# Optimization experiments

Measured on AMD Instinct MI355X. Metric: run time of the kernel, lower is better.

Reference implementation:

```python
import jax, jax.numpy as jnp
import numpy as np

WS = 7            # window size
NUM_HEADS = 16
DIM = 512
B_ = 4096         # num_windows * batch
NW = 1024         # windows per image
N = WS * WS


def _relative_position_index(ws=WS):
    # static int index table, computed exactly as in the torch module
    coords = np.stack(np.meshgrid(np.arange(ws), np.arange(ws), indexing='ij'))  # (2, ws, ws)
    coords = coords.reshape(2, -1)                                               # (2, N)
    rel = coords[:, :, None] - coords[:, None, :]                                # (2, N, N)
    rel = rel.transpose(1, 2, 0).astype(np.int64)                                # (N, N, 2)
    rel[:, :, 0] += ws - 1
    rel[:, :, 1] += ws - 1
    rel[:, :, 0] *= 2 * ws - 1
    return jnp.asarray(rel.sum(-1))                                              # (N, N)


def setup_inputs() -> dict:
    key = jax.random.key(0)
    ks = jax.random.split(key, 12)
    C = DIM
    std = 0.02
    inp = {
        'local_features': jax.random.normal(ks[0], (B_, N, C), jnp.float32),
        'global_features': jax.random.normal(ks[1], (B_, N, C), jnp.float32),
        'mask': jnp.zeros((NW, N, N), jnp.float32),  # 0/-inf shifted-window mask (all-visible here)
        'bias_table': std * jax.random.normal(ks[2], ((2 * WS - 1) * (2 * WS - 1), NUM_HEADS), jnp.float32),
        'Wk': std * jax.random.normal(ks[3], (C, C), jnp.float32),
        'bk': jnp.zeros((C,), jnp.float32),
        'Wq': std * jax.random.normal(ks[4], (C, C), jnp.float32),
        'bq': jnp.zeros((C,), jnp.float32),
        'Wv': std * jax.random.normal(ks[5], (C, C), jnp.float32),
        'bv': jnp.zeros((C,), jnp.float32),
        'Wp': std * jax.random.normal(ks[6], (C, C), jnp.float32),
        'bp': jnp.zeros((C,), jnp.float32),
    }
    return inp


def reference(local_features, global_features, mask, bias_table,
              Wk, bk, Wq, bq, Wv, bv, Wp, bp):
    Bw, n, C = local_features.shape
    h = NUM_HEADS
    d = C // h
    scale = d ** -0.5

    def heads(x, W, b):
        # torch Linear: x @ W.T + b ; then (B_, N, h, d) -> (B_, h, N, d)
        y = jnp.einsum('bnc,oc->bno', x, W) + b
        return y.reshape(Bw, n, h, d).transpose(0, 2, 1, 3)

    k = heads(local_features, Wk, bk)
    q = heads(global_features, Wq, bq) * scale
    v = heads(local_features, Wv, bv)

    attn = jnp.einsum('bhnd,bhmd->bhnm', q, k)                    # (B_, h, N, N)

    idx = _relative_position_index()                               # (N, N) static
    rpb = bias_table[idx]                                          # (N, N, h)
    attn = attn + rpb.transpose(2, 0, 1)[None]                     # add (1, h, N, N)

    nW = mask.shape[0]
    attn = attn.reshape(Bw // nW, nW, h, n, n) + mask[None, :, None]
    attn = attn.reshape(Bw, h, n, n)
    attn = jax.nn.softmax(attn, axis=-1)

    x = jnp.einsum('bhnm,bhmd->bnhd', attn, v).reshape(Bw, n, C)
    x = jnp.einsum('bnc,oc->bno', x, Wp) + bp
    return x
```

## Files before the change

### kernel.cpp

```cpp
#include <hip/hip_runtime.h>
#include <hip/hip_bf16.h>

typedef __hip_bfloat16 bf16;
typedef __attribute__((ext_vector_type(4))) float f32x4;
typedef __attribute__((ext_vector_type(8))) short short8;
typedef __attribute__((ext_vector_type(4))) short short4v;

#define NEGBIG (-3.0e38f)

__device__ __forceinline__ unsigned short f2b(float x) {
  union { float f; unsigned int u; } v; v.f = x;
  unsigned int r = v.u + 0x7fffu + ((v.u >> 16) & 1u);
  return (unsigned short)(r >> 16);
}

__device__ __forceinline__ void gl16(const void* g, void* l) {
  __builtin_amdgcn_global_load_lds(
      (const __attribute__((address_space(1))) unsigned int*)g,
      (__attribute__((address_space(3))) unsigned int*)l, 16, 0, 0);
}

__device__ __forceinline__ int xcd_swz(int orig, int nwg) {
  const int q = nwg >> 3, r = nwg & 7;
  const int xcd = orig & 7;
  const int base = (xcd < r) ? xcd * (q + 1) : r * (q + 1) + (xcd - r) * q;
  return base + (orig >> 3);
}

__global__ __launch_bounds__(256) void cvt_w_kernel(
    const float* __restrict__ a, const float* __restrict__ b,
    const float* __restrict__ c, const float* __restrict__ d,
    bf16* __restrict__ dst) {
  const int t = blockIdx.x * 256 + threadIdx.x;
  const float* srcs[4] = {a, b, c, d};
#pragma unroll
  for (int w = 0; w < 4; ++w) {
    const f32x4 v = *(const f32x4*)(srcs[w] + (size_t)t * 4);
    short4v o;
    o[0] = (short)f2b(v[0]); o[1] = (short)f2b(v[1]);
    o[2] = (short)f2b(v[2]); o[3] = (short)f2b(v[3]);
    *(short4v*)((short*)dst + (size_t)w * 262144 + (size_t)t * 4) = o;
  }
}

__global__ __launch_bounds__(256) void cvt_a(const float* __restrict__ src,
                                             short* __restrict__ dst, int M) {
  const int g = blockIdx.x * 256 + threadIdx.x;
  const int row = g >> 6, k8 = g & 63;
  if (row >= M) return;
  const float* sp = src + (size_t)row * 512 + k8 * 8;
  const f32x4 lo = *(const f32x4*)sp;
  const f32x4 hi = *(const f32x4*)(sp + 4);
  short8 u;
  u[0] = (short)f2b(lo[0]); u[1] = (short)f2b(lo[1]);
  u[2] = (short)f2b(lo[2]); u[3] = (short)f2b(lo[3]);
  u[4] = (short)f2b(hi[0]); u[5] = (short)f2b(hi[1]);
  u[6] = (short)f2b(hi[2]); u[7] = (short)f2b(hi[3]);
  *(short8*)(dst + (size_t)row * 512 + k8 * 8) = u;
}

__global__ __launch_bounds__(256) void prep_rpbL(const float* __restrict__ btab,
                                                 float* __restrict__ rpbL) {
  const int g = blockIdx.x * 256 + threadIdx.x;
  const int lane = g & 63, mn = (g >> 6) & 15, h = g >> 10;
  const int m = mn >> 2, n = mn & 3, l15 = lane & 15, lg = lane >> 4;
  const int cc = n * 16 + l15;
  const int aj = cc / 7, bj = cc % 7;
  f32x4 o;
#pragma unroll
  for (int reg = 0; reg < 4; ++reg) {
    const int i = m * 16 + lg * 4 + reg;
    if (i < 49 && cc < 49) {
      const int t = (i / 7 - aj + 6) * 13 + (i % 7 - bj + 6);
      o[reg] = btab[t * 16 + h];
    } else {
      o[reg] = NEGBIG;
    }
  }
  ((f32x4*)rpbL)[g] = o;
}

__global__ __launch_bounds__(256) void prep_maskL(const float* __restrict__ mask,
                                                  float* __restrict__ maskL) {
  const int g = blockIdx.x * 256 + threadIdx.x;
  const int lane = g & 63, mn = (g >> 6) & 15, wm = g >> 10;
  const int m = mn >> 2, n = mn & 3, l15 = lane & 15, lg = lane >> 4;
  const int cc = n * 16 + l15;
  f32x4 o;
#pragma unroll
  for (int reg = 0; reg < 4; ++reg) {
    const int i = m * 16 + lg * 4 + reg;
    o[reg] = (i < 49 && cc < 49) ? mask[(size_t)wm * 2401 + i * 49 + cc] : 0.f;
  }
  ((f32x4*)maskL)[g] = o;
}

__device__ __forceinline__ void stage_m97(const char* Ab, const char* Bb,
                                          char* As, char* Bs, int arow0,
                                          int brow0, int k0) {
  const int tid = threadIdx.x;
#pragma unroll
  for (int i = 0; i < 2; ++i) {
    const int s = tid + 512 * i;
    const int row = s >> 3;
    const int sc = (s & 7) ^ (row & 7);
    gl16(Ab + (size_t)(arow0 + row) * 1024 + k0 * 2 + sc * 16, As + s * 16);
  }
#pragma unroll
  for (int i = 0; i < 4; ++i) {
    const int s = tid + 512 * i;
    const int row = s >> 3;
    const int sc = (s & 7) ^ (row & 7);
    gl16(Bb + (size_t)(brow0 + row) * 1024 + k0 * 2 + sc * 16, Bs + s * 16);
  }
}

__global__ __launch_bounds__(512, 4) void gemm_kqv(
    const short* __restrict__ Al, const short* __restrict__ Ag,
    const short* __restrict__ wbf, const float* __restrict__ bk,
    const float* __restrict__ bq, const float* __restrict__ bv, float qscale,
    bf16* __restrict__ k_ws, bf16* __restrict__ q_ws, bf16* __restrict__ vT_ws,
    int M) {
  __shared__ char lds[49152];
  char* As = lds;
  char* Bs = lds + 16384;
  const int nwg = gridDim.x;
  const int t0 = xcd_swz(blockIdx.x, nwg);
  const int bn = t0 % 6, bm = t0 / 6;
  const int cls = bn >> 1, bnl = bn & 1;
  const int tid = threadIdx.x, lane = tid & 63, wid = tid >> 6;
  const int l15 = lane & 15, lg = lane >> 4;
  const bool swap = (cls == 2);
  const int wr = swap ? (wid & 3) : (wid >> 2);
  const int wc = swap ? (wid >> 2) : (wid & 3);
  const char* Ab = (const char*)((cls == 1) ? Ag : Al);
  const char* Bb = (const char*)(wbf + (size_t)cls * 262144);

  f32x4 acc[4][4];
#pragma unroll
  for (int m = 0; m < 4; ++m)
#pragma unroll
    for (int n = 0; n < 4; ++n) acc[m][n] = (f32x4){0.f, 0.f, 0.f, 0.f};

  const char* fam = swap ? Bs : As;
  const char* fbm = swap ? As : Bs;

  for (int kt = 0; kt < 8; ++kt) {
    stage_m97(Ab, Bb, As, Bs, bm * 128, bnl * 256, kt * 64);
    __syncthreads();
#pragma unroll
    for (int s = 0; s < 2; ++s) {
      short8 af[4], bfr[4];
#pragma unroll
      for (int m = 0; m < 4; ++m) {
        const int r = wr * 64 + m * 16 + l15;
        af[m] = *(const short8*)(fam + r * 128 +
                                 (((s * 4 + lg) ^ (r & 7)) << 4));
      }
#pragma unroll
      for (int n = 0; n < 4; ++n) {
        const int r = wc * 64 + n * 16 + l15;
        bfr[n] = *(const short8*)(fbm + r * 128 +
                                  (((s * 4 + lg) ^ (r & 7)) << 4));
      }
#pragma unroll
      for (int m = 0; m < 4; ++m)
#pragma unroll
        for (int n = 0; n < 4; ++n)
          acc[m][n] = __builtin_amdgcn_mfma_f32_16x16x32_bf16(
              af[m], bfr[n], acc[m][n], 0, 0, 0);
    }
    __syncthreads();
  }

  if (cls == 2) {
#pragma unroll
    for (int m = 0; m < 4; ++m) {
#pragma unroll
      for (int n = 0; n < 4; ++n) {
        const int tok = bm * 128 + wc * 64 + n * 16 + l15;
        if (tok < M) {
          const int w = tok / 49, nt = tok - w * 49;
#pragma unroll
          for (int reg = 0; reg < 4; ++reg) {
            const int ch = bnl * 256 + wr * 64 + m * 16 + lg * 4 + reg;
            const float v = acc[m][n][reg] + bv[ch];
            const int hh = ch >> 5, dd = ch & 31;
            vT_ws[(((size_t)w * 16 + hh) * 32 + dd) * 64 + nt] =
                __float2bfloat16(v);
          }
        }
      }
    }
  } else {
    const float* bb = (cls == 0) ? bk : bq;
    bf16* dp = (cls == 0) ? k_ws : q_ws;
    const float sc = (cls == 0) ? 1.0f : qscale;
#pragma unroll
    for (int m = 0; m < 4; ++m) {
#pragma unroll
      for (int n = 0; n < 4; ++n) {
        const int c = bnl * 256 + wc * 64 + n * 16 + l15;
        const float bvv = bb[c];
        const int hh = c >> 5, dd = c & 31;
#pragma unroll
        for (int reg = 0; reg < 4; ++reg) {
          const int r = bm * 128 + wr * 64 + m * 16 + lg * 4 + reg;
          if (r < M) {
            const int w = r / 49, nt = r - w * 49;
            dp[(((size_t)w * 16 + hh) * 49 + nt) * 32 + dd] =
                __float2bfloat16((acc[m][n][reg] + bvv) * sc);
          }
        }
      }
    }
  }
}

__global__ __launch_bounds__(512, 4) void gemm_p(const short* __restrict__ Abf,
                                                 const short* __restrict__ Bbf,
                                                 const float* __restrict__ bias,
                                                 float* __restrict__ dst,
                                                 int M) {
  __shared__ char lds[49152];
  char* As = lds;
  char* Bs = lds + 16384;
  const int nwg = gridDim.x;
  const int t0 = xcd_swz(blockIdx.x, nwg);
  const int bnl = t0 & 1, bm = t0 >> 1;
  const int tid = threadIdx.x, lane = tid & 63, wid = tid >> 6;
  const int wr = wid >> 2, wc = wid & 3, l15 = lane & 15, lg = lane >> 4;

  f32x4 acc[4][4];
#pragma unroll
  for (int m = 0; m < 4; ++m)
#pragma unroll
    for (int n = 0; n < 4; ++n) acc[m][n] = (f32x4){0.f, 0.f, 0.f, 0.f};

  for (int kt = 0; kt < 8; ++kt) {
    stage_m97((const char*)Abf, (const char*)Bbf, As, Bs, bm * 128, bnl * 256,
              kt * 64);
    __syncthreads();
#pragma unroll
    for (int s = 0; s < 2; ++s) {
      short8 af[4], bfr[4];
#pragma unroll
      for (int m = 0; m < 4; ++m) {
        const int r = wr * 64 + m * 16 + l15;
        af[m] = *(const short8*)(As + r * 128 +
                                 (((s * 4 + lg) ^ (r & 7)) << 4));
      }
#pragma unroll
      for (int n = 0; n < 4; ++n) {
        const int r = wc * 64 + n * 16 + l15;
        bfr[n] = *(const short8*)(Bs + r * 128 +
                                  (((s * 4 + lg) ^ (r & 7)) << 4));
      }
#pragma unroll
      for (int m = 0; m < 4; ++m)
#pragma unroll
        for (int n = 0; n < 4; ++n)
          acc[m][n] = __builtin_amdgcn_mfma_f32_16x16x32_bf16(
              af[m], bfr[n], acc[m][n], 0, 0, 0);
    }
    __syncthreads();
  }

#pragma unroll
  for (int m = 0; m < 4; ++m) {
#pragma unroll
    for (int n = 0; n < 4; ++n) {
      const int c = bnl * 256 + wc * 64 + n * 16 + l15;
      const float bvv = bias[c];
#pragma unroll
      for (int reg = 0; reg < 4; ++reg) {
        const int r = bm * 128 + wr * 64 + m * 16 + lg * 4 + reg;
        if (r < M) dst[(size_t)r * 512 + c] = acc[m][n][reg] + bvv;
      }
    }
  }
}

__global__ __launch_bounds__(256) void attn_win2(
    const bf16* __restrict__ q_ws, const bf16* __restrict__ k_ws,
    const bf16* __restrict__ vT_ws, const float* __restrict__ rpbL,
    const float* __restrict__ maskL, bf16* __restrict__ x_ws, int wstart) {
  __shared__ short sP[4][4096];
  const int tid = threadIdx.x, lane = tid & 63, wid = tid >> 6;
  const int l15 = lane & 15, lg = lane >> 4;
  const int wl = blockIdx.x;
  const int h = blockIdx.y * 4 + wid;
  const int wg = wstart + wl;
  char* Pl = (char*)sP[wid];
  const size_t base = ((size_t)wl * 16 + h) * 1568;
  const short8 z8 = (short8){0, 0, 0, 0, 0, 0, 0, 0};

  short8 qf[4], kf[4];
#pragma unroll
  for (int m = 0; m < 4; ++m) {
    const int r = m * 16 + l15;
    qf[m] = (r < 49) ? *(const short8*)(q_ws + base + r * 32 + lg * 8) : z8;
    kf[m] = (r < 49) ? *(const short8*)(k_ws + base + r * 32 + lg * 8) : z8;
  }
  f32x4 lc[4][4];
#pragma unroll
  for (int m = 0; m < 4; ++m)
#pragma unroll
    for (int n = 0; n < 4; ++n)
      lc[m][n] = __builtin_amdgcn_mfma_f32_16x16x32_bf16(
          qf[m], kf[n], (f32x4){0.f, 0.f, 0.f, 0.f}, 0, 0, 0);

  const f32x4* rbp = (const f32x4*)rpbL + (size_t)h * 1024 + lane;
  const f32x4* mkp = (const f32x4*)maskL + (size_t)(wg & 1023) * 1024 + lane;
#pragma unroll
  for (int m = 0; m < 4; ++m)
#pragma unroll
    for (int n = 0; n < 4; ++n) {
      const int mn = m * 4 + n;
      lc[m][n] += rbp[mn * 64] + mkp[mn * 64];
    }

#pragma unroll
  for (int m = 0; m < 4; ++m) {
#pragma unroll
    for (int reg = 0; reg < 4; ++reg) {
      float vmax = fmaxf(fmaxf(lc[m][0][reg], lc[m][1][reg]),
                         fmaxf(lc[m][2][reg], lc[m][3][reg]));
#pragma unroll
      for (int off = 1; off < 16; off <<= 1)
        vmax = fmaxf(vmax, __shfl_xor(vmax, off, 64));
      float e[4], ssum = 0.f;
#pragma unroll
      for (int n = 0; n < 4; ++n) {
        e[n] = __expf(lc[m][n][reg] - vmax);
        ssum += e[n];
      }
#pragma unroll
      for (int off = 1; off < 16; off <<= 1) ssum += __shfl_xor(ssum, off, 64);
      const float inv = __builtin_amdgcn_rcpf(ssum);
      const int i = m * 16 + lg * 4 + reg;
#pragma unroll
      for (int n = 0; n < 4; ++n) {
        const int cc = n * 16 + l15;
        *(unsigned short*)(Pl + i * 128 + ((2 * cc) ^ ((i & 7) << 4))) =
            f2b(e[n] * inv);
      }
    }
  }

  f32x4 xacc[4][2];
#pragma unroll
  for (int m = 0; m < 4; ++m)
#pragma unroll
    for (int n = 0; n < 2; ++n) xacc[m][n] = (f32x4){0.f, 0.f, 0.f, 0.f};
  const size_t vbase = ((size_t)wl * 16 + h) * 2048;
#pragma unroll
  for (int s = 0; s < 2; ++s) {
    short8 pf[4], vf[2];
#pragma unroll
    for (int m = 0; m < 4; ++m) {
      const int i = m * 16 + l15;
      pf[m] = *(const short8*)(Pl + i * 128 +
                               ((s * 64 + lg * 16) ^ ((i & 7) << 4)));
    }
#pragma unroll
    for (int n = 0; n < 2; ++n) {
      const int dd = n * 16 + l15;
      short8 vv = *(const short8*)(vT_ws + vbase + dd * 64 + s * 32 + lg * 8);
      if (s == 1) {
        if (lg == 3) vv = z8;
        else if (lg == 2) {
          vv[1] = 0; vv[2] = 0; vv[3] = 0; vv[4] = 0;
          vv[5] = 0; vv[6] = 0; vv[7] = 0;
        }
      }
      vf[n] = vv;
    }
#pragma unroll
    for (int m = 0; m < 4; ++m)
#pragma unroll
      for (int n = 0; n < 2; ++n)
        xacc[m][n] = __builtin_amdgcn_mfma_f32_16x16x32_bf16(
            pf[m], vf[n], xacc[m][n], 0, 0, 0);
  }

#pragma unroll
  for (int m = 0; m < 4; ++m)
#pragma unroll
    for (int n = 0; n < 2; ++n)
#pragma unroll
      for (int reg = 0; reg < 4; ++reg) {
        const int i = m * 16 + lg * 4 + reg;
        const int dd = n * 16 + l15;
        *(unsigned short*)(Pl + i * 80 + ((2 * dd) ^ ((i & 3) << 4))) =
            f2b(xacc[m][n][reg]);
      }
#pragma unroll
  for (int g = 0; g < 4; ++g) {
    const int row = g * 16 + (lane >> 2);
    if (row < 49) {
      const short8 xv = *(const short8*)(
          Pl + row * 80 + (((lane & 3) * 16) ^ ((row & 3) << 4)));
      *(short8*)(x_ws + ((size_t)wl * 49 + row) * 512 + h * 32 +
                 (lane & 3) * 8) = xv;
    }
  }
}

extern "C" void kernel_launch(void* const* d_in, const int* in_sizes, int n_in,
                              void* d_out, int out_size, void* d_ws,
                              size_t ws_size, hipStream_t stream) {
  const float* lf   = (const float*)d_in[0];
  const float* gfx  = (const float*)d_in[1];
  const float* mask = (const float*)d_in[2];
  const float* btab = (const float*)d_in[3];
  const float* Wk = (const float*)d_in[4];  const float* bk = (const float*)d_in[5];
  const float* Wq = (const float*)d_in[6];  const float* bq = (const float*)d_in[7];
  const float* Wv = (const float*)d_in[8];  const float* bv = (const float*)d_in[9];
  const float* Wp = (const float*)d_in[10]; const float* bp = (const float*)d_in[11];
  float* out = (float*)d_out;

  char* ws = (char*)d_ws;
  short* wbf = (short*)ws;
  size_t off = (size_t)4 * 262144 * 2;
  float* rpbL = (float*)(ws + off); off += (size_t)16 * 4096 * 4;
  float* maskL = (float*)(ws + off); off += (size_t)1024 * 4096 * 4;

  const size_t perw = 2 * 49 * 1024 + 2 * 50176 + 65536;
  size_t avail = (ws_size > off + 65536) ? ws_size - off - 65536 : 0;
  int CH = (int)((avail > 300000) ? (avail - 262144) / perw : 1);
  if (CH > 4096) CH = 4096;
  if (CH < 1) CH = 1;
  const int RWS = ((CH * 49 + 127) / 128) * 128;

  short* Al = (short*)(ws + off); off += (size_t)RWS * 1024;
  short* Ag = (short*)(ws + off); off += (size_t)RWS * 1024;
  bf16* q_ws = (bf16*)(ws + off); off += (size_t)CH * 50176;
  bf16* k_ws = (bf16*)(ws + off); off += (size_t)CH * 50176;
  bf16* vT_ws = (bf16*)(ws + off); off += (size_t)CH * 65536;
  bf16* x_ws = (bf16*)Al;

  cvt_w_kernel<<<256, 256, 0, stream>>>(Wk, Wq, Wv, Wp, (bf16*)wbf);
  prep_rpbL<<<64, 256, 0, stream>>>(btab, rpbL);
  prep_maskL<<<4096, 256, 0, stream>>>(mask, maskL);

  const float qscale = 0.17677669529663687f;
  for (int wstart = 0; wstart < 4096; wstart += CH) {
    const int nwin = (4096 - wstart < CH) ? (4096 - wstart) : CH;
    const int M = nwin * 49;
    const int gy = (M + 127) / 128;
    const int cg = (M * 64 + 255) / 256;
    cvt_a<<<cg, 256, 0, stream>>>(lf + (size_t)wstart * 25088, Al, M);
    cvt_a<<<cg, 256, 0, stream>>>(gfx + (size_t)wstart * 25088, Ag, M);
    gemm_kqv<<<6 * gy, 512, 0, stream>>>(Al, Ag, wbf, bk, bq, bv, qscale,
                                         k_ws, q_ws, vT_ws, M);
    attn_win2<<<dim3(nwin, 4), 256, 0, stream>>>(q_ws, k_ws, vT_ws, rpbL,
                                                 maskL, x_ws, wstart);
    gemm_p<<<2 * gy, 512, 0, stream>>>((const short*)x_ws, wbf + 3 * 262144,
                                       bp, out + (size_t)wstart * 25088, M);
  }
}
```

Before: 1.271 ms.

## Fuse fp32-to-bf16 activation conversion into the QKV GEMM staging

Drops the separate cvt_a passes over local and global features. The QKV GEMM now loads fp32 activation tiles into LDS, converts them to bf16 with packed convert instructions, and writes them into the swizzled layout before running the MFMA loop. This removes a full write and read of bf16 copies of both inputs through global memory. In exchange, LDS per block grows to 80KB, each k-step gains an extra barrier, and each activation tile is re-read and re-converted by all six column blocks.

```diff
diff --git a/kernel.cpp b/kernel.cpp
--- a/kernel.cpp
+++ b/kernel.cpp
@@ -41,22 +41,6 @@
     o[2] = (short)f2b(v[2]); o[3] = (short)f2b(v[3]);
     *(short4v*)((short*)dst + (size_t)w * 262144 + (size_t)t * 4) = o;
   }
-}
-
-__global__ __launch_bounds__(256) void cvt_a(const float* __restrict__ src,
-                                             short* __restrict__ dst, int M) {
-  const int g = blockIdx.x * 256 + threadIdx.x;
-  const int row = g >> 6, k8 = g & 63;
-  if (row >= M) return;
-  const float* sp = src + (size_t)row * 512 + k8 * 8;
-  const f32x4 lo = *(const f32x4*)sp;
-  const f32x4 hi = *(const f32x4*)(sp + 4);
-  short8 u;
-  u[0] = (short)f2b(lo[0]); u[1] = (short)f2b(lo[1]);
-  u[2] = (short)f2b(lo[2]); u[3] = (short)f2b(lo[3]);
-  u[4] = (short)f2b(hi[0]); u[5] = (short)f2b(hi[1]);
-  u[6] = (short)f2b(hi[2]); u[7] = (short)f2b(hi[3]);
-  *(short8*)(dst + (size_t)row * 512 + k8 * 8) = u;
 }
 
 __global__ __launch_bounds__(256) void prep_rpbL(const float* __restrict__ btab,
@@ -95,35 +79,16 @@
   ((f32x4*)maskL)[g] = o;
 }
 
-__device__ __forceinline__ void stage_m97(const char* Ab, const char* Bb,
-                                          char* As, char* Bs, int arow0,
-                                          int brow0, int k0) {
-  const int tid = threadIdx.x;
-#pragma unroll
-  for (int i = 0; i < 2; ++i) {
-    const int s = tid + 512 * i;
-    const int row = s >> 3;
-    const int sc = (s & 7) ^ (row & 7);
-    gl16(Ab + (size_t)(arow0 + row) * 1024 + k0 * 2 + sc * 16, As + s * 16);
-  }
-#pragma unroll
-  for (int i = 0; i < 4; ++i) {
-    const int s = tid + 512 * i;
-    const int row = s >> 3;
-    const int sc = (s & 7) ^ (row & 7);
-    gl16(Bb + (size_t)(brow0 + row) * 1024 + k0 * 2 + sc * 16, Bs + s * 16);
-  }
-}
-
 __global__ __launch_bounds__(512, 4) void gemm_kqv(
-    const short* __restrict__ Al, const short* __restrict__ Ag,
+    const float* __restrict__ lf, const float* __restrict__ gfx,
     const short* __restrict__ wbf, const float* __restrict__ bk,
     const float* __restrict__ bq, const float* __restrict__ bv, float qscale,
     bf16* __restrict__ k_ws, bf16* __restrict__ q_ws, bf16* __restrict__ vT_ws,
     int M) {
-  __shared__ char lds[49152];
-  char* As = lds;
-  char* Bs = lds + 16384;
+  __shared__ char lds[81920];
+  char* Af32 = lds;
+  char* Abf = lds + 32768;
+  char* Bs = lds + 49152;
   const int nwg = gridDim.x;
   const int t0 = xcd_swz(blockIdx.x, nwg);
   const int bn = t0 % 6, bm = t0 / 6;
@@ -133,7 +98,7 @@
   const bool swap = (cls == 2);
   const int wr = swap ? (wid & 3) : (wid >> 2);
   const int wc = swap ? (wid >> 2) : (wid & 3);
-  const char* Ab = (const char*)((cls == 1) ? Ag : Al);
+  const float* Af = (cls == 1) ? gfx : lf;
   const char* Bb = (const char*)(wbf + (size_t)cls * 262144);
 
   f32x4 acc[4][4];
@@ -142,12 +107,46 @@
 #pragma unroll
     for (int n = 0; n < 4; ++n) acc[m][n] = (f32x4){0.f, 0.f, 0.f, 0.f};
 
-  const char* fam = swap ? Bs : As;
-  const char* fbm = swap ? As : Bs;
+  const char* fam = swap ? Bs : Abf;
+  const char* fbm = swap ? Abf : Bs;
+
+  const int crow0 = tid >> 4;
+  const int ccol = tid & 15;
+  const int c4 = ccol >> 1, hh8 = (ccol & 1) * 8;
 
   for (int kt = 0; kt < 8; ++kt) {
-    stage_m97(Ab, Bb, As, Bs, bm * 128, bnl * 256, kt * 64);
+    const int k0 = kt * 64;
+#pragma unroll
+    for (int i = 0; i < 4; ++i) {
+      const int s = tid + 512 * i;
+      const int row = s >> 4, col = s & 15;
+      int gr = bm * 128 + row;
+      if (gr >= M) gr = M - 1;
+      gl16((const char*)Af + (size_t)gr * 2048 + k0 * 4 + col * 16,
+           Af32 + s * 16);
+    }
+#pragma unroll
+    for (int i = 0; i < 4; ++i) {
+      const int s = tid + 512 * i;
+      const int row = s >> 3;
+      const int sc = (s & 7) ^ (row & 7);
+      gl16(Bb + (size_t)(bnl * 256 + row) * 1024 + k0 * 2 + sc * 16,
+           Bs + s * 16);
+    }
     __syncthreads();
+
+#pragma unroll
+    for (int j = 0; j < 4; ++j) {
+      const int rj = crow0 + 32 * j;
+      const f32x4 v = *(const f32x4*)(Af32 + (tid + 512 * j) * 16);
+      unsigned int w0, w1;
+      asm("v_cvt_pk_bf16_f32 %0, %1, %2" : "=v"(w0) : "v"(v[0]), "v"(v[1]));
+      asm("v_cvt_pk_bf16_f32 %0, %1, %2" : "=v"(w1) : "v"(v[2]), "v"(v[3]));
+      *(unsigned long long*)(Abf + rj * 128 + (((c4 ^ (rj & 7)) << 4) | hh8)) =
+          ((unsigned long long)w1 << 32) | w0;
+    }
+    __syncthreads();
+
 #pragma unroll
     for (int s = 0; s < 2; ++s) {
       short8 af[4], bfr[4];
@@ -214,6 +213,26 @@
         }
       }
     }
+  }
+}
+
+__device__ __forceinline__ void stage_m97(const char* Ab, const char* Bb,
+                                          char* As, char* Bs, int arow0,
+                                          int brow0, int k0) {
+  const int tid = threadIdx.x;
+#pragma unroll
+  for (int i = 0; i < 2; ++i) {
+    const int s = tid + 512 * i;
+    const int row = s >> 3;
+    const int sc = (s & 7) ^ (row & 7);
+    gl16(Ab + (size_t)(arow0 + row) * 1024 + k0 * 2 + sc * 16, As + s * 16);
+  }
+#pragma unroll
+  for (int i = 0; i < 4; ++i) {
+    const int s = tid + 512 * i;
+    const int row = s >> 3;
+    const int sc = (s & 7) ^ (row & 7);
+    gl16(Bb + (size_t)(brow0 + row) * 1024 + k0 * 2 + sc * 16, Bs + s * 16);
   }
 }
 
@@ -426,19 +445,16 @@
   float* rpbL = (float*)(ws + off); off += (size_t)16 * 4096 * 4;
   float* maskL = (float*)(ws + off); off += (size_t)1024 * 4096 * 4;
 
-  const size_t perw = 2 * 49 * 1024 + 2 * 50176 + 65536;
+  const size_t perw = 50176 + 2 * 50176 + 65536;
   size_t avail = (ws_size > off + 65536) ? ws_size - off - 65536 : 0;
-  int CH = (int)((avail > 300000) ? (avail - 262144) / perw : 1);
+  int CH = (int)(avail / perw);
   if (CH > 4096) CH = 4096;
   if (CH < 1) CH = 1;
-  const int RWS = ((CH * 49 + 127) / 128) * 128;
-
-  short* Al = (short*)(ws + off); off += (size_t)RWS * 1024;
-  short* Ag = (short*)(ws + off); off += (size_t)RWS * 1024;
+
+  bf16* x_ws = (bf16*)(ws + off); off += (size_t)CH * 50176;
   bf16* q_ws = (bf16*)(ws + off); off += (size_t)CH * 50176;
   bf16* k_ws = (bf16*)(ws + off); off += (size_t)CH * 50176;
   bf16* vT_ws = (bf16*)(ws + off); off += (size_t)CH * 65536;
-  bf16* x_ws = (bf16*)Al;
 
   cvt_w_kernel<<<256, 256, 0, stream>>>(Wk, Wq, Wv, Wp, (bf16*)wbf);
   prep_rpbL<<<64, 256, 0, stream>>>(btab, rpbL);
@@ -449,11 +465,10 @@
     const int nwin = (4096 - wstart < CH) ? (4096 - wstart) : CH;
     const int M = nwin * 49;
     const int gy = (M + 127) / 128;
-    const int cg = (M * 64 + 255) / 256;
-    cvt_a<<<cg, 256, 0, stream>>>(lf + (size_t)wstart * 25088, Al, M);
-    cvt_a<<<cg, 256, 0, stream>>>(gfx + (size_t)wstart * 25088, Ag, M);
-    gemm_kqv<<<6 * gy, 512, 0, stream>>>(Al, Ag, wbf, bk, bq, bv, qscale,
-                                         k_ws, q_ws, vT_ws, M);
+    gemm_kqv<<<6 * gy, 512, 0, stream>>>(lf + (size_t)wstart * 25088,
+                                         gfx + (size_t)wstart * 25088, wbf,
+                                         bk, bq, bv, qscale, k_ws, q_ws,
+                                         vT_ws, M);
     attn_win2<<<dim3(nwin, 4), 256, 0, stream>>>(q_ws, k_ws, vT_ws, rpbL,
                                                  maskL, x_ws, wstart);
     gemm_p<<<2 * gy, 512, 0, stream>>>((const short*)x_ws, wbf + 3 * 262144,
```

New measurement: 1.161 ms. -8.7%, faster.
